# Kernel tuning notes

Hardware: AMD Instinct MI355X
Metric: run time of the kernel (lower is better)

Reference implementation:

```python
import jax, jax.numpy as jnp
import numpy as np

N_NEWS = 200000
N_COMPANIES = 10000
N_EDGES = 640000
HIDDEN = 256


def setup_inputs() -> dict:
    key = jax.random.key(0)
    ks = jax.random.split(key, 7)
    scale = 1.0 / np.sqrt(HIDDEN)  # keep tanh out of full saturation
    news_x = jax.random.normal(ks[0], (N_NEWS, HIDDEN), dtype=jnp.float32)
    company_x = jax.random.normal(ks[1], (N_COMPANIES, HIDDEN), dtype=jnp.float32)
    W_news = jax.random.normal(ks[2], (HIDDEN, HIDDEN), dtype=jnp.float32) * scale
    W_company = jax.random.normal(ks[3], (HIDDEN, HIDDEN), dtype=jnp.float32) * scale
    v = jax.random.normal(ks[4], (HIDDEN,), dtype=jnp.float32) * scale
    src = jax.random.randint(ks[5], (N_EDGES,), 0, N_NEWS, dtype=jnp.int64)
    dst = jax.random.randint(ks[6], (N_EDGES,), 0, N_COMPANIES, dtype=jnp.int64)
    return {
        "news_x": news_x,
        "company_x": company_x,
        "W_news": W_news,
        "W_company": W_company,
        "v": v,
        "src": src,
        "dst": dst,
        "num_companies": N_COMPANIES,
    }


def reference(news_x, company_x, W_news, W_company, v, src, dst, num_companies):
    # Gather per-edge endpoint features, project (nn.Linear applies x @ W.T).
    news_part = news_x[src] @ W_news.T          # [E, H]
    company_part = company_x[dst] @ W_company.T  # [E, H]
    scores = jnp.tanh(news_part + company_part) @ v  # [E]

    # Segment-wise (per-company) numerically stable softmax over incoming edges.
    smax = jax.ops.segment_max(scores, dst, num_segments=num_companies)  # [C]
    scores_exp = jnp.exp(scores - smax[dst])                             # [E]
    denom = jax.ops.segment_sum(scores_exp, dst, num_segments=num_companies)[dst]
    weights = scores_exp / jnp.clip(denom, 1e-9)                         # [E]

    # Weighted scatter-add of raw news features into company slots.
    out = jax.ops.segment_sum(news_x[src] * weights[:, None], dst,
                              num_segments=num_companies)               # [C, H]
    return out
```

## Files before the change

### kernel.cpp

```cpp
#include <hip/hip_runtime.h>
#include <hip/hip_bf16.h>
#include <cmath>
#include <cstdint>


#define H 256

typedef __attribute__((ext_vector_type(8))) short bfrag;
typedef __attribute__((ext_vector_type(4))) float ffrag;

__device__ __forceinline__ ushort f2bf(float f) {
  uint u = __float_as_uint(f);
  uint r = u + 0x7FFFu + ((u >> 16) & 1u);
  return (ushort)(r >> 16);
}
__device__ __forceinline__ float bf2f(ushort h) {
  return __uint_as_float((uint)h << 16);
}

__global__ void prep_kernel(const float* __restrict__ Wn, const float* __restrict__ Wc,
                            ushort* __restrict__ WnHi, ushort* __restrict__ WnLo,
                            ushort* __restrict__ WcHi, ushort* __restrict__ WcLo,
                            const int* __restrict__ dst, int* __restrict__ counts, int E) {
  const int b = blockIdx.x, tid = threadIdx.x;
  if (b < 256) {
    int i = b * 256 + tid;
    float w = Wn[i];
    ushort h = f2bf(w);
    WnHi[i] = h;
    WnLo[i] = f2bf(w - bf2f(h));
  } else if (b < 512) {
    int i = (b - 256) * 256 + tid;
    float w = Wc[i];
    ushort h = f2bf(w);
    WcHi[i] = h;
    WcLo[i] = f2bf(w - bf2f(h));
  } else {
    int e = (b - 512) * 256 + tid;
    if (e < E) atomicAdd(&counts[dst[e]], 1);
  }
}

__global__ void scan_kernel(const int* __restrict__ counts, int* __restrict__ offsets,
                            int* __restrict__ cursor, int C) {
  __shared__ int wsum[16];
  int tid = threadIdx.x;
  int lane = tid & 63, wid = tid >> 6;
  int base = 0;
  for (int start = 0; start < C; start += 1024) {
    int idx = start + tid;
    int val = (idx < C) ? counts[idx] : 0;
    int x = val;
#pragma unroll
    for (int off = 1; off < 64; off <<= 1) {
      int y = __shfl_up(x, off);
      if (lane >= off) x += y;
    }
    if (lane == 63) wsum[wid] = x;
    __syncthreads();
    int add = base;
    for (int w = 0; w < wid; ++w) add += wsum[w];
    if (idx < C) {
      int excl = add + x - val;
      offsets[idx] = excl;
      cursor[idx]  = excl;
    }
    int tot = 0;
#pragma unroll
    for (int w = 0; w < 16; ++w) tot += wsum[w];
    __syncthreads();
    base += tot;
  }
  if (tid == 0) offsets[C] = base;
}

__global__ void fill_kernel(const int* __restrict__ src, const int* __restrict__ dst,
                            int* __restrict__ cursor, int* __restrict__ srcs_sorted, int E) {
  int e = blockIdx.x * blockDim.x + threadIdx.x;
  if (e < E) {
    int d = dst[e];
    int pos = atomicAdd(&cursor[d], 1);
    srcs_sorted[pos] = src[e];
  }
}

__global__ __launch_bounds__(512, 2) void gemm_persist(
    const float* __restrict__ Xc, const ushort* __restrict__ WcHi,
    const ushort* __restrict__ WcLo, ushort* __restrict__ cproj, int MC, int GC,
    const float* __restrict__ Xn, const ushort* __restrict__ WnHi,
    const ushort* __restrict__ WnLo, ushort* __restrict__ nproj,
    ushort* __restrict__ nxbf, int MN) {
  constexpr int PITCH = 264;
  __shared__ ushort Xs[2][64 * PITCH];
  const int tid = threadIdx.x;
  const int wv = tid >> 6, lane = tid & 63;
  const int q = lane >> 4, nidx = lane & 15;
  const int GN = gridDim.x - GC;

  const float* X; const ushort *Whi, *Wlo; ushort *proj, *xb; int M, nb, lb;
  if ((int)blockIdx.x < GC) {
    X = Xc; Whi = WcHi; Wlo = WcLo; proj = cproj; xb = nullptr; M = MC;
    nb = GC; lb = blockIdx.x;
  } else {
    X = Xn; Whi = WnHi; Wlo = WnLo; proj = nproj; xb = nxbf; M = MN;
    nb = GN; lb = blockIdx.x - GC;
  }
  const int nt = (M + 63) >> 6;
  const int qt = nt / nb, rt = nt % nb;
  const int first = lb * qt + (lb < rt ? lb : rt);
  const int cnt = qt + (lb < rt ? 1 : 0);
  if (cnt <= 0) return;

  bfrag bhi[8][2], blo[8][2];
#pragma unroll
  for (int ks = 0; ks < 8; ++ks)
#pragma unroll
    for (int tt = 0; tt < 2; ++tt) {
      const size_t off = (size_t)(wv * 32 + tt * 16 + nidx) * H + ks * 32 + q * 8;
      bhi[ks][tt] = *(const bfrag*)(Whi + off);
      blo[ks][tt] = *(const bfrag*)(Wlo + off);
    }

  float4 xr[8];
  auto load8 = [&](int tile) {
#pragma unroll
    for (int j = 0; j < 8; ++j) {
      const int flat = j * 2048 + tid * 4;
      int gr = tile * 64 + (flat >> 8);
      if (gr >= M) gr = M - 1;
      xr[j] = *(const float4*)(X + (size_t)gr * H + (flat & 255));
    }
  };
  auto writebuf = [&](int p, int tile) {
#pragma unroll
    for (int j = 0; j < 8; ++j) {
      const int flat = j * 2048 + tid * 4;
      const int r = flat >> 8, k = flat & 255;
      ushort4 b4;
      b4.x = f2bf(xr[j].x); b4.y = f2bf(xr[j].y);
      b4.z = f2bf(xr[j].z); b4.w = f2bf(xr[j].w);
      *(ushort4*)&Xs[p][r * PITCH + k] = b4;
      if (xb) {
        const int gr = tile * 64 + r;
        *(ushort4*)(xb + (size_t)gr * H + k) = b4;
      }
    }
  };

  load8(first);
  writebuf(0, first);
  int p = 0;
  for (int t = 0; t < cnt; ++t) {
    __syncthreads();
    const int tile = first + t;
    const bool more = (t + 1 < cnt);
    if (more) load8(tile + 1);

    ffrag acc[4][2];
#pragma unroll
    for (int i = 0; i < 4; ++i) { acc[i][0] = (ffrag)(0.f); acc[i][1] = (ffrag)(0.f); }
#pragma unroll
    for (int ks = 0; ks < 8; ++ks) {
      bfrag a[4];
#pragma unroll
      for (int i = 0; i < 4; ++i)
        a[i] = *(const bfrag*)&Xs[p][(16 * i + nidx) * PITCH + ks * 32 + q * 8];
#pragma unroll
      for (int i = 0; i < 4; ++i)
#pragma unroll
        for (int tt = 0; tt < 2; ++tt) {
          acc[i][tt] = __builtin_amdgcn_mfma_f32_16x16x32_bf16(a[i], bhi[ks][tt], acc[i][tt], 0, 0, 0);
          acc[i][tt] = __builtin_amdgcn_mfma_f32_16x16x32_bf16(a[i], blo[ks][tt], acc[i][tt], 0, 0, 0);
        }
    }

    const int row0 = tile * 64;
#pragma unroll
    for (int i = 0; i < 4; ++i)
#pragma unroll
      for (int r = 0; r < 4; ++r) {
        const int grow = row0 + 16 * i + q * 4 + r;
        if (grow < M) {
#pragma unroll
          for (int tt = 0; tt < 2; ++tt)
            proj[(size_t)grow * H + wv * 32 + tt * 16 + nidx] = f2bf(acc[i][tt][r]);
        }
      }

    if (more) writebuf(p ^ 1, tile + 1);
    p ^= 1;
  }
}

__device__ __forceinline__ float fast_tanh(float x) {
  float e = __builtin_amdgcn_exp2f(x * 2.8853900817779268f);
  float t = __builtin_amdgcn_rcpf(e + 1.f);
  return __builtin_fmaf(-2.f, t, 1.f);
}

__global__ __launch_bounds__(256) void edge_flash_kernel(
    const ushort* __restrict__ news_projbf, const ushort* __restrict__ company_projbf,
    const float* __restrict__ v, const int* __restrict__ offsets,
    const int* __restrict__ srcs, const ushort* __restrict__ news_xbf,
    float* __restrict__ out) {
  const int c = blockIdx.x;
  const int tid = threadIdx.x;
  const int sl = tid & 31;
  const int hw = tid >> 5;
  __shared__ float cp[H];
  __shared__ float mW[8], lW[8];
  __shared__ float OW[8][H];
  cp[tid] = bf2f(company_projbf[(size_t)c * H + tid]);
  __syncthreads();
  const float4 va = *(const float4*)(v + sl * 8);
  const float4 vb = *(const float4*)(v + sl * 8 + 4);
  const float4 ca = *(const float4*)&cp[sl * 8];
  const float4 cb = *(const float4*)&cp[sl * 8 + 4];
  const float vv[8] = {va.x, va.y, va.z, va.w, vb.x, vb.y, vb.z, vb.w};
  const float cq[8] = {ca.x, ca.y, ca.z, ca.w, cb.x, cb.y, cb.z, cb.w};
  const int beg = offsets[c], end = offsets[c + 1];

  float m = -INFINITY, l = 0.f;
  float O[8] = {0.f, 0.f, 0.f, 0.f, 0.f, 0.f, 0.f, 0.f};

  int i = beg + hw;
  if (i < end) {
    int s = srcs[i];
    bfrag pr = *(const bfrag*)(news_projbf + (size_t)s * H + sl * 8);
    bfrag xr = *(const bfrag*)(news_xbf + (size_t)s * H + sl * 8);
    for (;;) {
      const int inext = i + 8;
      const bool more = (inext < end);
      bfrag prn, xrn;
      if (more) {
        int sn = srcs[inext];
        prn = *(const bfrag*)(news_projbf + (size_t)sn * H + sl * 8);
        xrn = *(const bfrag*)(news_xbf + (size_t)sn * H + sl * 8);
      }
      float r = 0.f;
#pragma unroll
      for (int j = 0; j < 8; ++j)
        r += fast_tanh(bf2f((ushort)pr[j]) + cq[j]) * vv[j];
#pragma unroll
      for (int off = 16; off > 0; off >>= 1) r += __shfl_xor(r, off);
      const float mnew = fmaxf(m, r);
      const float alpha = __expf(m - mnew);
      const float pa = __expf(r - mnew);
      l = l * alpha + pa;
#pragma unroll
      for (int j = 0; j < 8; ++j)
        O[j] = O[j] * alpha + pa * bf2f((ushort)xr[j]);
      m = mnew;
      i = inext;
      if (!more) break;
      pr = prn; xr = xrn;
    }
  }

  if (sl == 0) { mW[hw] = m; lW[hw] = l; }
  float4 oa = make_float4(O[0], O[1], O[2], O[3]);
  float4 ob = make_float4(O[4], O[5], O[6], O[7]);
  *(float4*)&OW[hw][sl * 8] = oa;
  *(float4*)&OW[hw][sl * 8 + 4] = ob;
  __syncthreads();
  float mstar = -INFINITY;
#pragma unroll
  for (int w = 0; w < 8; ++w) mstar = fmaxf(mstar, mW[w]);
  float denom = 0.f, val = 0.f;
#pragma unroll
  for (int w = 0; w < 8; ++w) {
    const float sc = (lW[w] > 0.f) ? __expf(mW[w] - mstar) : 0.f;
    denom += lW[w] * sc;
    val += OW[w][tid] * sc;
  }
  out[(size_t)c * H + tid] = val / fmaxf(denom, 1e-9f);
}

extern "C" void kernel_launch(void* const* d_in, const int* in_sizes, int n_in,
                              void* d_out, int out_size, void* d_ws, size_t ws_size,
                              hipStream_t stream) {
  const float* news_x    = (const float*)d_in[0];
  const float* company_x = (const float*)d_in[1];
  const float* W_news    = (const float*)d_in[2];
  const float* W_company = (const float*)d_in[3];
  const float* v         = (const float*)d_in[4];
  const int*   src       = (const int*)d_in[5];
  const int*   dst       = (const int*)d_in[6];
  const int N = in_sizes[0] / H;
  const int C = in_sizes[1] / H;
  const int E = in_sizes[5];
  float* out = (float*)d_out;

  char* p = (char*)d_ws;
  ushort* news_projbf    = (ushort*)p; p += (size_t)N * H * sizeof(ushort);
  ushort* news_xbf       = (ushort*)p; p += (size_t)N * H * sizeof(ushort);
  ushort* company_projbf = (ushort*)p; p += (size_t)C * H * sizeof(ushort);
  int*    srcs_sorted    = (int*)p;    p += (size_t)E * sizeof(int);
  ushort* Wn_hi          = (ushort*)p; p += (size_t)H * H * sizeof(ushort);
  ushort* Wn_lo          = (ushort*)p; p += (size_t)H * H * sizeof(ushort);
  ushort* Wc_hi          = (ushort*)p; p += (size_t)H * H * sizeof(ushort);
  ushort* Wc_lo          = (ushort*)p; p += (size_t)H * H * sizeof(ushort);
  int*    counts         = (int*)p;    p += (size_t)C * sizeof(int);
  int*    offsets        = (int*)p;    p += (size_t)(C + 1) * sizeof(int);
  int*    cursor         = (int*)p;    p += (size_t)C * sizeof(int);

  hipMemsetAsync(counts, 0, (size_t)C * sizeof(int), stream);
  prep_kernel<<<512 + (E + 255) / 256, 256, 0, stream>>>(
      W_news, W_company, Wn_hi, Wn_lo, Wc_hi, Wc_lo, dst, counts, E);
  scan_kernel<<<1, 1024, 0, stream>>>(counts, offsets, cursor, C);
  fill_kernel<<<(E + 255) / 256, 256, 0, stream>>>(src, dst, cursor, srcs_sorted, E);

  const int GC = 24, GN = 488;
  gemm_persist<<<GC + GN, 512, 0, stream>>>(
      company_x, Wc_hi, Wc_lo, company_projbf, C, GC,
      news_x, Wn_hi, Wn_lo, news_projbf, news_xbf, N);

  edge_flash_kernel<<<C, 256, 0, stream>>>(news_projbf, company_projbf, v, offsets,
                                           srcs_sorted, news_xbf, out);
}
```

Baseline: 534.3 us.

## Stage GEMM output through LDS for coalesced stores, unroll edge loop by two

The persistent GEMM now writes its bf16 accumulator tile into the shared-memory buffer and then copies it out in 16-byte row-contiguous chunks, replacing scattered 2-byte global stores. This adds two block barriers per tile, and the next tile's prefetch now starts after the staging write. The edge kernel handles two edges per iteration, with two-deep prefetch and one combined online-softmax update, to expose more memory-level parallelism. The persistent grid is halved, so each block processes more tiles.

```diff
diff --git a/kernel.cpp b/kernel.cpp
--- a/kernel.cpp
+++ b/kernel.cpp
@@ -174,20 +174,29 @@
         }
     }
 
+    __syncthreads();
     const int row0 = tile * 64;
 #pragma unroll
     for (int i = 0; i < 4; ++i)
 #pragma unroll
-      for (int r = 0; r < 4; ++r) {
-        const int grow = row0 + 16 * i + q * 4 + r;
-        if (grow < M) {
-#pragma unroll
-          for (int tt = 0; tt < 2; ++tt)
-            proj[(size_t)grow * H + wv * 32 + tt * 16 + nidx] = f2bf(acc[i][tt][r]);
+      for (int tt = 0; tt < 2; ++tt)
+#pragma unroll
+        for (int r = 0; r < 4; ++r)
+          Xs[p][(16 * i + q * 4 + r) * PITCH + wv * 32 + tt * 16 + nidx] =
+              f2bf(acc[i][tt][r]);
+    if (more) writebuf(p ^ 1, tile + 1);
+    __syncthreads();
+    {
+      const int r = tid >> 3, k0 = (tid & 7) * 32;
+      const int grow = row0 + r;
+      if (grow < M) {
+#pragma unroll
+        for (int jj = 0; jj < 4; ++jj) {
+          bfrag t8 = *(const bfrag*)&Xs[p][r * PITCH + k0 + jj * 8];
+          *(bfrag*)(proj + (size_t)grow * H + k0 + jj * 8) = t8;
         }
       }
-
-    if (more) writebuf(p ^ 1, tile + 1);
+    }
     p ^= 1;
   }
 }
@@ -225,43 +234,64 @@
 
   int i = beg + hw;
   if (i < end) {
-    int s = srcs[i];
-    bfrag pr = *(const bfrag*)(news_projbf + (size_t)s * H + sl * 8);
-    bfrag xr = *(const bfrag*)(news_xbf + (size_t)s * H + sl * 8);
+    bfrag pr0, xr0, pr1 = (bfrag)(short)0, xr1 = (bfrag)(short)0;
+    {
+      const int s = srcs[i];
+      pr0 = *(const bfrag*)(news_projbf + (size_t)s * H + sl * 8);
+      xr0 = *(const bfrag*)(news_xbf + (size_t)s * H + sl * 8);
+    }
+    bool has1 = (i + 8 < end);
+    if (has1) {
+      const int s = srcs[i + 8];
+      pr1 = *(const bfrag*)(news_projbf + (size_t)s * H + sl * 8);
+      xr1 = *(const bfrag*)(news_xbf + (size_t)s * H + sl * 8);
+    }
     for (;;) {
-      const int inext = i + 8;
-      const bool more = (inext < end);
-      bfrag prn, xrn;
-      if (more) {
-        int sn = srcs[inext];
-        prn = *(const bfrag*)(news_projbf + (size_t)sn * H + sl * 8);
-        xrn = *(const bfrag*)(news_xbf + (size_t)sn * H + sl * 8);
-      }
-      float r = 0.f;
+      const int j0 = i + 16;
+      const bool m0 = has1 && (j0 < end);
+      const bool m1 = m0 && (j0 + 8 < end);
+      bfrag npr0 = (bfrag)(short)0, nxr0 = (bfrag)(short)0;
+      bfrag npr1 = (bfrag)(short)0, nxr1 = (bfrag)(short)0;
+      if (m0) {
+        const int s = srcs[j0];
+        npr0 = *(const bfrag*)(news_projbf + (size_t)s * H + sl * 8);
+        nxr0 = *(const bfrag*)(news_xbf + (size_t)s * H + sl * 8);
+      }
+      if (m1) {
+        const int s = srcs[j0 + 8];
+        npr1 = *(const bfrag*)(news_projbf + (size_t)s * H + sl * 8);
+        nxr1 = *(const bfrag*)(news_xbf + (size_t)s * H + sl * 8);
+      }
+      float r0 = 0.f, r1 = 0.f;
+#pragma unroll
+      for (int j = 0; j < 8; ++j) {
+        r0 += fast_tanh(bf2f((ushort)pr0[j]) + cq[j]) * vv[j];
+        r1 += fast_tanh(bf2f((ushort)pr1[j]) + cq[j]) * vv[j];
+      }
+#pragma unroll
+      for (int off = 16; off > 0; off >>= 1) {
+        r0 += __shfl_xor(r0, off);
+        r1 += __shfl_xor(r1, off);
+      }
+      if (!has1) r1 = -INFINITY;
+      const float mnew = fmaxf(m, fmaxf(r0, r1));
+      const float alpha = __expf(m - mnew);
+      const float p0 = __expf(r0 - mnew);
+      const float p1 = has1 ? __expf(r1 - mnew) : 0.f;
+      l = l * alpha + p0 + p1;
 #pragma unroll
       for (int j = 0; j < 8; ++j)
-        r += fast_tanh(bf2f((ushort)pr[j]) + cq[j]) * vv[j];
-#pragma unroll
-      for (int off = 16; off > 0; off >>= 1) r += __shfl_xor(r, off);
-      const float mnew = fmaxf(m, r);
-      const float alpha = __expf(m - mnew);
-      const float pa = __expf(r - mnew);
-      l = l * alpha + pa;
-#pragma unroll
-      for (int j = 0; j < 8; ++j)
-        O[j] = O[j] * alpha + pa * bf2f((ushort)xr[j]);
+        O[j] = O[j] * alpha + p0 * bf2f((ushort)xr0[j]) + p1 * bf2f((ushort)xr1[j]);
       m = mnew;
-      i = inext;
-      if (!more) break;
-      pr = prn; xr = xrn;
+      if (!m0) break;
+      i = j0; has1 = m1;
+      pr0 = npr0; xr0 = nxr0; pr1 = npr1; xr1 = nxr1;
     }
   }
 
   if (sl == 0) { mW[hw] = m; lW[hw] = l; }
-  float4 oa = make_float4(O[0], O[1], O[2], O[3]);
-  float4 ob = make_float4(O[4], O[5], O[6], O[7]);
-  *(float4*)&OW[hw][sl * 8] = oa;
-  *(float4*)&OW[hw][sl * 8 + 4] = ob;
+  *(float4*)&OW[hw][sl * 8]     = make_float4(O[0], O[1], O[2], O[3]);
+  *(float4*)&OW[hw][sl * 8 + 4] = make_float4(O[4], O[5], O[6], O[7]);
   __syncthreads();
   float mstar = -INFINITY;
 #pragma unroll
@@ -310,7 +340,7 @@
   scan_kernel<<<1, 1024, 0, stream>>>(counts, offsets, cursor, C);
   fill_kernel<<<(E + 255) / 256, 256, 0, stream>>>(src, dst, cursor, srcs_sorted, E);
 
-  const int GC = 24, GN = 488;
+  const int GC = 12, GN = 244;
   gemm_persist<<<GC + GN, 512, 0, stream>>>(
       company_x, Wc_hi, Wc_lo, company_projbf, C, GC,
       news_x, Wn_hi, Wn_lo, news_projbf, news_xbf, N);
```

Result: no change. 543.7 us (+1.8%).
